# Performance work log

Hardware: AMD Instinct MI355X
Metric: run time of the kernel (lower is better)

Reference implementation:

```python
import jax, jax.numpy as jnp
import numpy as np

N_QUBITS = 10


def setup_inputs() -> dict:
    key = jax.random.key(0)
    kx, kw = jax.random.split(key)
    # x: batch of rotation angles, last dim = n_qubits
    x = jax.random.normal(kx, (16384, 256, N_QUBITS), dtype=jnp.float32)
    # trainable per-qubit RY angles (nn.Parameter in the torch module)
    weights = jax.random.normal(kw, (N_QUBITS,), dtype=jnp.float32)
    return {"x": x, "weights": weights}


def reference(x, weights):
    """Exact analytic evaluation of the quantum circuit.

    Circuit: RX(x_i) on wire i, RY(w_i) on wire i, CNOT chain (0,1),(1,2),...,
    then expval(PauliZ(i)) on each wire.

    Derivation: pulling Z_i back through the CNOT chain (CNOT(c,t)^† Z_t
    CNOT(c,t) = Z_c Z_t) gives <Z_i> = <Z_0 Z_1 ... Z_i>. The pre-CNOT state
    is a product state, and for a single qubit RY(w)RX(x)|0> has
    <Z> = cos(x) cos(w). Hence out[..., i] = prod_{j<=i} cos(x_j) cos(w_j),
    i.e. a cumulative product along the qubit axis. This is bit-exact with
    the full state-vector simulation (up to float rounding).
    """
    per_qubit = jnp.cos(x) * jnp.cos(weights)  # [..., n_qubits], weights broadcast
    return jnp.cumprod(per_qubit, axis=-1)      # [..., n_qubits]
```

## Files before the change

kernel.cpp:

```cpp
#include <hip/hip_runtime.h>


#define BLOCK 256
#define ROWS_PER_THREAD 2
#define ROWS_PER_BLOCK (BLOCK * ROWS_PER_THREAD)
#define NQ 10
#define WORDS_PER_BLOCK (ROWS_PER_BLOCK * NQ)
#define U4_PER_BLOCK (WORDS_PER_BLOCK / 4)
#define U4_PER_THREAD (U4_PER_BLOCK / BLOCK)

__global__ __launch_bounds__(BLOCK) void qcircuit_kernel(
    const float* __restrict__ x,
    const float* __restrict__ w,
    float* __restrict__ out,
    int n_rows)
{
    __shared__ float4 buf4[U4_PER_BLOCK];
    float* bufw = (float*)buf4;

    const int tid = threadIdx.x;
    const long long block_row0 = (long long)blockIdx.x * ROWS_PER_BLOCK;
    const long long total_u4   = ((long long)n_rows * NQ) / 4;
    const long long u4_base    = (long long)blockIdx.x * U4_PER_BLOCK;
    const float4* __restrict__ gin  = (const float4*)x;
    float4* __restrict__       gout = (float4*)out;

    #pragma unroll
    for (int k = 0; k < U4_PER_THREAD; ++k) {
        long long gi = u4_base + (long long)(k * BLOCK + tid);
        if (gi < total_u4) buf4[k * BLOCK + tid] = gin[gi];
    }

    float cw[NQ];
    #pragma unroll
    for (int j = 0; j < NQ; ++j) cw[j] = __cosf(w[j]);

    __syncthreads();

    #pragma unroll
    for (int m = 0; m < ROWS_PER_THREAD; ++m) {
        const int r = tid + m * BLOCK;
        if (block_row0 + r < n_rows) {
            float v[NQ];
            #pragma unroll
            for (int j = 0; j < NQ; ++j) v[j] = bufw[r * NQ + j];
            float p = 1.0f;
            #pragma unroll
            for (int j = 0; j < NQ; ++j) {
                p *= __cosf(v[j]) * cw[j];
                v[j] = p;
            }
            #pragma unroll
            for (int j = 0; j < NQ; ++j) bufw[r * NQ + j] = v[j];
        }
    }

    __syncthreads();

    #pragma unroll
    for (int k = 0; k < U4_PER_THREAD; ++k) {
        long long gi = u4_base + (long long)(k * BLOCK + tid);
        if (gi < total_u4) gout[gi] = buf4[k * BLOCK + tid];
    }
}

extern "C" void kernel_launch(void* const* d_in, const int* in_sizes, int n_in,
                              void* d_out, int out_size, void* d_ws, size_t ws_size,
                              hipStream_t stream) {
    const float* x = (const float*)d_in[0];
    const float* w = (const float*)d_in[1];
    float* out = (float*)d_out;

    const int n_elem = in_sizes[0];
    const int n_rows = n_elem / NQ;
    const int blocks = (n_rows + ROWS_PER_BLOCK - 1) / ROWS_PER_BLOCK;

    hipLaunchKernelGGL(qcircuit_kernel, dim3(blocks), dim3(BLOCK), 0, stream,
                       x, w, out, n_rows);
}
```

Baseline: 284.9 us.

## Give each thread contiguous rows, swizzle LDS, store directly with nontemporal writes

```diff
diff --git a/kernel.cpp b/kernel.cpp
--- a/kernel.cpp
+++ b/kernel.cpp
@@ -1,34 +1,35 @@
 #include <hip/hip_runtime.h>
 
 
+typedef float vf4 __attribute__((ext_vector_type(4)));
+
 #define BLOCK 256
+#define NQ 10
 #define ROWS_PER_THREAD 2
 #define ROWS_PER_BLOCK (BLOCK * ROWS_PER_THREAD)
-#define NQ 10
-#define WORDS_PER_BLOCK (ROWS_PER_BLOCK * NQ)
-#define U4_PER_BLOCK (WORDS_PER_BLOCK / 4)
-#define U4_PER_THREAD (U4_PER_BLOCK / BLOCK)
+#define F4_PER_BLOCK (ROWS_PER_BLOCK * NQ / 4)
+#define F4_PER_THREAD (F4_PER_BLOCK / BLOCK)
+#define SWZ(L) ((L) + ((L) >> 3))
+#define LDS_F4 (SWZ(F4_PER_BLOCK - 1) + 1)
 
 __global__ __launch_bounds__(BLOCK) void qcircuit_kernel(
     const float* __restrict__ x,
     const float* __restrict__ w,
     float* __restrict__ out,
-    int n_rows)
+    long long n_rows)
 {
-    __shared__ float4 buf4[U4_PER_BLOCK];
-    float* bufw = (float*)buf4;
+    __shared__ vf4 lds[LDS_F4];
 
     const int tid = threadIdx.x;
-    const long long block_row0 = (long long)blockIdx.x * ROWS_PER_BLOCK;
-    const long long total_u4   = ((long long)n_rows * NQ) / 4;
-    const long long u4_base    = (long long)blockIdx.x * U4_PER_BLOCK;
-    const float4* __restrict__ gin  = (const float4*)x;
-    float4* __restrict__       gout = (float4*)out;
+    const long long total_f4 = (n_rows * NQ) / 4;
+    const long long f4_base  = (long long)blockIdx.x * F4_PER_BLOCK;
+    const vf4* __restrict__ gin = (const vf4*)x;
 
     #pragma unroll
-    for (int k = 0; k < U4_PER_THREAD; ++k) {
-        long long gi = u4_base + (long long)(k * BLOCK + tid);
-        if (gi < total_u4) buf4[k * BLOCK + tid] = gin[gi];
+    for (int k = 0; k < F4_PER_THREAD; ++k) {
+        const int L = k * BLOCK + tid;
+        const long long gi = f4_base + L;
+        if (gi < total_f4) lds[SWZ(L)] = gin[gi];
     }
 
     float cw[NQ];
@@ -37,30 +38,33 @@
 
     __syncthreads();
 
+    float f[4 * F4_PER_THREAD];
     #pragma unroll
-    for (int m = 0; m < ROWS_PER_THREAD; ++m) {
-        const int r = tid + m * BLOCK;
-        if (block_row0 + r < n_rows) {
-            float v[NQ];
-            #pragma unroll
-            for (int j = 0; j < NQ; ++j) v[j] = bufw[r * NQ + j];
-            float p = 1.0f;
-            #pragma unroll
-            for (int j = 0; j < NQ; ++j) {
-                p *= __cosf(v[j]) * cw[j];
-                v[j] = p;
-            }
-            #pragma unroll
-            for (int j = 0; j < NQ; ++j) bufw[r * NQ + j] = v[j];
-        }
+    for (int k = 0; k < F4_PER_THREAD; ++k) {
+        const vf4 v = lds[SWZ(tid * F4_PER_THREAD + k)];
+        f[4 * k + 0] = v.x; f[4 * k + 1] = v.y;
+        f[4 * k + 2] = v.z; f[4 * k + 3] = v.w;
     }
 
-    __syncthreads();
+    float p0 = 1.0f, p1 = 1.0f;
+    #pragma unroll
+    for (int j = 0; j < NQ; ++j) {
+        p0 *= __cosf(f[j]) * cw[j];
+        f[j] = p0;
+        p1 *= __cosf(f[NQ + j]) * cw[j];
+        f[NQ + j] = p1;
+    }
 
+    const long long word_base = f4_base * 4 + (long long)tid * (NQ * ROWS_PER_THREAD);
+    vf4* __restrict__ gout = (vf4*)(out + word_base);
     #pragma unroll
-    for (int k = 0; k < U4_PER_THREAD; ++k) {
-        long long gi = u4_base + (long long)(k * BLOCK + tid);
-        if (gi < total_u4) gout[gi] = buf4[k * BLOCK + tid];
+    for (int k = 0; k < F4_PER_THREAD; ++k) {
+        if (word_base + 4 * k + 3 < n_rows * NQ) {
+            vf4 v;
+            v.x = f[4 * k + 0]; v.y = f[4 * k + 1];
+            v.z = f[4 * k + 2]; v.w = f[4 * k + 3];
+            __builtin_nontemporal_store(v, gout + k);
+        }
     }
 }
 
@@ -71,9 +75,8 @@
     const float* w = (const float*)d_in[1];
     float* out = (float*)d_out;
 
-    const int n_elem = in_sizes[0];
-    const int n_rows = n_elem / NQ;
-    const int blocks = (n_rows + ROWS_PER_BLOCK - 1) / ROWS_PER_BLOCK;
+    const long long n_rows = (long long)in_sizes[0] / NQ;
+    const int blocks = (int)((n_rows + ROWS_PER_BLOCK - 1) / ROWS_PER_BLOCK);
 
     hipLaunchKernelGGL(qcircuit_kernel, dim3(blocks), dim3(BLOCK), 0, stream,
                        x, w, out, n_rows);
```

After: 551.2 us. 93.5% more time.
